# Kernel optimization log

Measured on AMD Instinct MI355X. Metric: run time of the kernel, lower is better.

The kernel has to match this reference:

```python
import jax, jax.numpy as jnp
import numpy as np

NUM_LEVELS = 3
B, T, D, H = 512, 2048, 64, 32


def _uni(k, shape, fan_in):
    s = 1.0 / np.sqrt(fan_in)
    return jax.random.uniform(k, shape, jnp.float32, -s, s)


def setup_inputs() -> dict:
    key = jax.random.key(0)
    ks = jax.random.split(key, 10)
    lw = jnp.linspace(1.0, float(NUM_LEVELS), NUM_LEVELS)
    lw = lw / lw.sum()
    return {
        "latent_ys": jax.random.normal(ks[0], (B, T, D), jnp.float32),
        "Wx": _uni(ks[1], (D, H), D), "bx": _uni(ks[2], (H,), D),
        "Wu": _uni(ks[3], (D, H), D), "bu": _uni(ks[4], (H,), D),
        "Ws": _uni(ks[5], (2 * H, 1), 2 * H), "bs": _uni(ks[6], (1,), 2 * H),
        "level_weights": lw,
        "Wf": _uni(ks[7], (2 * D, D), 2 * D), "bf": _uni(ks[8], (D,), 2 * D),
        "gamma": jnp.ones((D,), jnp.float32),
        "beta": jnp.zeros((D,), jnp.float32),
    }


def reference(latent_ys, Wx, bx, Wu, bu, Ws, bs, level_weights, Wf, bf, gamma, beta):
    Bn, Tn, Dn = latent_ys.shape
    x_repr = latent_ys[:, 0, :]          # (B,D)
    u_repr = latent_ys.mean(axis=1)       # (B,D)

    # Eq. 8-9 attention: score_net is linear on concat, so S[i,j] = ex_i.w1 + eu_j.w2 + b
    ex = x_repr @ Wx + bx                 # (B,H)
    eu = u_repr @ Wu + bu                 # (B,H)
    Hn = ex.shape[-1]
    S = (ex @ Ws[:Hn, 0])[:, None] + (eu @ Ws[Hn:, 0])[None, :] + bs[0]
    eye = jnp.eye(Bn, dtype=bool)
    S = jnp.where(eye, -jnp.inf, S)
    weights = jax.nn.softmax(S, axis=-1)  # (B,B), diag = 0

    # pyramidal sort (Algorithm 1), vectorized over the batch dim
    other = ~eye
    active = other
    dt = latent_ys.dtype
    levels = []
    for _ in range(NUM_LEVELS - 1):
        cnt = active.sum(-1, keepdims=True).astype(dt)                         # (B,1)
        asum = jnp.sum(jnp.where(active, weights, 0.0), -1, keepdims=True)      # (B,1)
        mean_val = asum / jnp.maximum(cnt, 1.0)
        lower = active & (weights <= mean_val)                                  # (B,B)
        lcnt = lower.sum(-1).astype(dt)[:, None]                                # (B,1)
        lsum = lower.astype(dt) @ u_repr                                        # (B,D)
        levels.append(jnp.where(lcnt > 0, lsum / jnp.maximum(lcnt, 1.0), 0.0))
        active = active & ~lower
    acnt = active.sum(-1).astype(dt)[:, None]
    asum_r = active.astype(dt) @ u_repr
    top_idx = jnp.argmax(jnp.where(other, weights, -1.0), axis=-1)              # (B,)
    fallback = u_repr[top_idx]
    levels.append(jnp.where(acnt > 0, asum_r / jnp.maximum(acnt, 1.0), fallback))
    level_reprs = jnp.stack(levels, axis=1)                                     # (B,L,D)

    cross = jnp.einsum('bld,l->bd', level_reprs, level_weights)                 # (B,D)
    # fusion Linear on concat([latent_ys, cross]) split into two GEMMs
    fused = latent_ys @ Wf[:Dn] + (cross @ Wf[Dn:] + bf)[:, None, :]           # (B,T,D)
    y = fused + latent_ys
    mu = y.mean(-1, keepdims=True)
    var = y.var(-1, keepdims=True)
    return gamma * (y - mu) * jax.lax.rsqrt(var + 1e-5) + beta
```

## Files before the change

### kernel.cpp

```cpp
#include <hip/hip_runtime.h>

typedef unsigned short ushort_t;
typedef __attribute__((ext_vector_type(8))) short short8;
typedef __attribute__((ext_vector_type(4))) float f32x4;

#define BB 512
#define TT 2048
#define DD 64

__device__ __forceinline__ ushort_t f2b(float f) {
    union { float f; unsigned int i; } v; v.f = f;
    unsigned int u = v.i;
    unsigned int r = (u + 0x7fffu + ((u >> 16) & 1u)) >> 16;
    return (ushort_t)r;
}

__global__ __launch_bounds__(1024) void k_umean(const float* __restrict__ lat,
                                                const float* __restrict__ Wu,
                                                const float* __restrict__ Ws,
                                                float* __restrict__ u,
                                                float* __restrict__ bj,
                                                ushort_t* __restrict__ latb) {
    int b = blockIdx.x;
    int tid = threadIdx.x;
    int cg = tid & 15;
    int rs = tid >> 4;
    const float* base = lat + (size_t)b * TT * DD;
    ushort_t* bbase = latb + (size_t)b * TT * DD;
    float acc[4] = {0.f, 0.f, 0.f, 0.f};
#pragma unroll 4
    for (int k = 0; k < 32; k++) {
        int r = rs + 64 * k;
        float4 vv = *reinterpret_cast<const float4*>(base + (size_t)r * DD + cg * 4);
        acc[0] += vv.x; acc[1] += vv.y; acc[2] += vv.z; acc[3] += vv.w;
        ushort4 sv;
        sv.x = f2b(vv.x); sv.y = f2b(vv.y); sv.z = f2b(vv.z); sv.w = f2b(vv.w);
        *reinterpret_cast<ushort4*>(bbase + (size_t)r * DD + cg * 4) = sv;
    }
    __shared__ float sm[64][64];
#pragma unroll
    for (int j = 0; j < 4; j++) sm[rs][cg * 4 + j] = acc[j];
    __syncthreads();
    {
        int col = tid & 63, g = tid >> 6;
        float p = 0.0f;
#pragma unroll
        for (int k = 0; k < 4; k++) p += sm[g + 16 * k][col];
        sm[g][col] = p;
    }
    __syncthreads();
    if (tid < 64) {
        float tot = 0.0f;
#pragma unroll
        for (int g = 0; g < 16; g++) tot += sm[g][tid];
        float um = tot * (1.0f / (float)TT);
        u[(size_t)b * DD + tid] = um;
        float vv = 0.0f;
#pragma unroll
        for (int h = 0; h < 32; h++) vv += Wu[tid * 32 + h] * Ws[32 + h];
        float p = um * vv;
#pragma unroll
        for (int m = 1; m < 64; m <<= 1) p += __shfl_xor(p, m, 64);
        if (tid == 0) bj[b] = p;
    }
}

__global__ __launch_bounds__(256) void k_levels(const float* __restrict__ u,
                                                const float* __restrict__ bj,
                                                const float* __restrict__ lw,
                                                const float* __restrict__ Wf,
                                                const float* __restrict__ bfv,
                                                float* __restrict__ cbias) {
    int i = blockIdx.x;
    int tid = threadIdx.x;
    int lane = tid & 63, wv = tid >> 6;
    __shared__ signed char lvl[512];
    __shared__ float redf[16];
    __shared__ int redi[8];
    __shared__ __align__(16) float lr[16][3][64];
    __shared__ float crossS[64];

    int jA = tid, jB = tid + 256;
    float vA = bj[jA], vB = bj[jB];

    float mx; int mi;
    if (vB > vA) { mx = vB; mi = jB; } else { mx = vA; mi = jA; }
#pragma unroll
    for (int m = 1; m < 64; m <<= 1) {
        float om = __shfl_xor(mx, m, 64);
        int oi = __shfl_xor(mi, m, 64);
        if (om > mx || (om == mx && oi < mi)) { mx = om; mi = oi; }
    }
    if (lane == 0) { redf[wv] = mx; redi[wv] = mi; }
    __syncthreads();
    float maxb = redf[0]; int j1 = redi[0];
#pragma unroll
    for (int w2 = 1; w2 < 4; w2++) {
        float om = redf[w2]; int oi = redi[w2];
        if (om > maxb || (om == maxb && oi < j1)) { maxb = om; j1 = oi; }
    }

    float eA = expf(vA - maxb), eB = expf(vB - maxb);
    float zs = eA + eB;
    float mx2; int mi2;
    {
        float tA = (jA == j1) ? -3.4e38f : vA;
        float tB = (jB == j1) ? -3.4e38f : vB;
        if (tB > tA) { mx2 = tB; mi2 = jB; } else { mx2 = tA; mi2 = jA; }
    }
#pragma unroll
    for (int m = 1; m < 64; m <<= 1) {
        float om = __shfl_xor(mx2, m, 64);
        int oi = __shfl_xor(mi2, m, 64);
        if (om > mx2 || (om == mx2 && oi < mi2)) { mx2 = om; mi2 = oi; }
        zs += __shfl_xor(zs, m, 64);
    }
    if (lane == 0) { redf[4 + wv] = mx2; redi[4 + wv] = mi2; redf[8 + wv] = zs; }
    __syncthreads();
    float Z = redf[8] + redf[9] + redf[10] + redf[11];
    int j2 = redi[4]; float m2v = redf[4];
#pragma unroll
    for (int w2 = 1; w2 < 4; w2++) {
        float om = redf[4 + w2]; int oi = redi[4 + w2];
        if (om > m2v || (om == m2v && oi < j2)) { m2v = om; j2 = oi; }
    }

    float Ei = expf(bj[i] - maxb);
    float denom = Z - Ei;
    float wA = (jA == i) ? 0.0f : (eA / denom);
    float wB = (jB == i) ? 0.0f : (eB / denom);

    float s = wA + wB;
#pragma unroll
    for (int m = 1; m < 64; m <<= 1) s += __shfl_xor(s, m, 64);
    if (lane == 0) redf[wv] = s;
    __syncthreads();
    float mean0 = (redf[0] + redf[1] + redf[2] + redf[3]) * (1.0f / 511.0f);

    float pa = 0.0f, ca = 0.0f, c1 = 0.0f;
    if (jA != i) { if (wA <= mean0) c1 += 1.0f; else { pa += wA; ca += 1.0f; } }
    if (jB != i) { if (wB <= mean0) c1 += 1.0f; else { pa += wB; ca += 1.0f; } }
#pragma unroll
    for (int m = 1; m < 64; m <<= 1) {
        pa += __shfl_xor(pa, m, 64);
        ca += __shfl_xor(ca, m, 64);
        c1 += __shfl_xor(c1, m, 64);
    }
    if (lane == 0) { redf[4 + wv] = pa; redf[8 + wv] = ca; redf[12 + wv] = c1; }
    __syncthreads();
    float asum1 = redf[4] + redf[5] + redf[6] + redf[7];
    float cact  = redf[8] + redf[9] + redf[10] + redf[11];
    float cnt1  = redf[12] + redf[13] + redf[14] + redf[15];
    float mean1 = asum1 / fmaxf(cact, 1.0f);

    float c2 = 0.0f;
    signed char lA, lB;
    if (jA == i) lA = -1;
    else if (wA <= mean0) lA = 0;
    else if (wA <= mean1) { lA = 1; c2 += 1.0f; }
    else lA = 2;
    if (jB == i) lB = -1;
    else if (wB <= mean0) lB = 0;
    else if (wB <= mean1) { lB = 1; c2 += 1.0f; }
    else lB = 2;
    lvl[jA] = lA; lvl[jB] = lB;
#pragma unroll
    for (int m = 1; m < 64; m <<= 1) c2 += __shfl_xor(c2, m, 64);
    if (lane == 0) redf[wv] = c2;
    __syncthreads();
    float cnt2 = redf[0] + redf[1] + redf[2] + redf[3];
    float cnt3 = cact - cnt2;

    int jg = tid >> 4;
    int d4 = (tid & 15) << 2;
    float4 a0 = make_float4(0.f, 0.f, 0.f, 0.f);
    float4 a1 = make_float4(0.f, 0.f, 0.f, 0.f);
    float4 a2 = make_float4(0.f, 0.f, 0.f, 0.f);
#pragma unroll 8
    for (int j = jg; j < 512; j += 16) {
        int l = lvl[j];
        float4 uv = *reinterpret_cast<const float4*>(u + (size_t)j * DD + d4);
        if (l == 0) { a0.x += uv.x; a0.y += uv.y; a0.z += uv.z; a0.w += uv.w; }
        else if (l == 1) { a1.x += uv.x; a1.y += uv.y; a1.z += uv.z; a1.w += uv.w; }
        else if (l == 2) { a2.x += uv.x; a2.y += uv.y; a2.z += uv.z; a2.w += uv.w; }
    }
    *reinterpret_cast<float4*>(&lr[jg][0][d4]) = a0;
    *reinterpret_cast<float4*>(&lr[jg][1][d4]) = a1;
    *reinterpret_cast<float4*>(&lr[jg][2][d4]) = a2;
    __syncthreads();

    if (tid < 64) {
        float s0 = 0.0f, s1 = 0.0f, s2 = 0.0f;
#pragma unroll
        for (int g2 = 0; g2 < 16; g2++) {
            s0 += lr[g2][0][tid];
            s1 += lr[g2][1][tid];
            s2 += lr[g2][2][tid];
        }
        int fb = (j1 == i) ? j2 : j1;
        float L1 = (cnt1 > 0.0f) ? s0 / cnt1 : 0.0f;
        float L2 = (cnt2 > 0.0f) ? s1 / cnt2 : 0.0f;
        float L3 = (cnt3 > 0.0f) ? s2 / cnt3 : u[(size_t)fb * DD + tid];
        crossS[tid] = lw[0] * L1 + lw[1] * L2 + lw[2] * L3;
    }
    __syncthreads();
    if (tid < 64) {
        int n = tid;
        float sacc = 0.0f;
        for (int dd = 0; dd < 64; dd++) sacc += crossS[dd] * Wf[(64 + dd) * 64 + n];
        cbias[(size_t)i * DD + n] = sacc + bfv[n];
    }
}

__global__ __launch_bounds__(256) void k_fused(const ushort_t* __restrict__ latb,
                                               const float* __restrict__ Wf,
                                               const float* __restrict__ cbias,
                                               const float* __restrict__ gamma,
                                               const float* __restrict__ beta,
                                               float* __restrict__ out) {
    int tid = threadIdx.x;
    int lane = tid & 63, wv = tid >> 6;
    int lo = lane & 15, quad = lane >> 4;
    long wid = (long)blockIdx.x * 4 + wv;

    short8 bfr[4][2];
#pragma unroll
    for (int c = 0; c < 4; c++) {
        int n = 16 * c + lo;
#pragma unroll
        for (int s = 0; s < 2; s++) {
            short8 t;
#pragma unroll
            for (int j = 0; j < 8; j++) {
                int k = 32 * s + 8 * quad + j;
                float vv = Wf[k * 64 + n] + (k == n ? 1.0f : 0.0f);
                t[j] = (short)f2b(vv);
            }
            bfr[c][s] = t;
        }
    }
    float ga[4], be[4], cb[4];
    int b = (int)(wid >> 5);
#pragma unroll
    for (int c = 0; c < 4; c++) {
        int n = 16 * c + lo;
        ga[c] = gamma[n];
        be[c] = beta[n];
        cb[c] = cbias[(size_t)b * DD + n];
    }

    for (int t4 = 0; t4 < 4; t4++) {
        long row0 = (wid * 4 + t4) * 16;
        const ushort_t* ap = latb + (size_t)(row0 + lo) * DD + quad * 8;
        short8 a0 = *reinterpret_cast<const short8*>(ap);
        short8 a1 = *reinterpret_cast<const short8*>(ap + 32);

        f32x4 acc[4];
#pragma unroll
        for (int c = 0; c < 4; c++) { acc[c] = (f32x4){0.f, 0.f, 0.f, 0.f}; }
#pragma unroll
        for (int c = 0; c < 4; c++) {
            acc[c] = __builtin_amdgcn_mfma_f32_16x16x32_bf16(a0, bfr[c][0], acc[c], 0, 0, 0);
            acc[c] = __builtin_amdgcn_mfma_f32_16x16x32_bf16(a1, bfr[c][1], acc[c], 0, 0, 0);
        }
        float y[4][4];
#pragma unroll
        for (int c = 0; c < 4; c++)
#pragma unroll
            for (int r = 0; r < 4; r++) y[c][r] = acc[c][r] + cb[c];
#pragma unroll
        for (int r = 0; r < 4; r++) {
            float s = y[0][r] + y[1][r] + y[2][r] + y[3][r];
            float q = y[0][r] * y[0][r] + y[1][r] * y[1][r] + y[2][r] * y[2][r] + y[3][r] * y[3][r];
#pragma unroll
            for (int m = 1; m < 16; m <<= 1) {
                s += __shfl_xor(s, m, 64);
                q += __shfl_xor(q, m, 64);
            }
            float mean = s * (1.0f / 64.0f);
            float var = q * (1.0f / 64.0f) - mean * mean;
            float rstd = rsqrtf(var + 1e-5f);
            long row = row0 + quad * 4 + r;
#pragma unroll
            for (int c = 0; c < 4; c++) {
                float o = ga[c] * (y[c][r] - mean) * rstd + be[c];
                out[(size_t)row * DD + 16 * c + lo] = o;
            }
        }
    }
}

extern "C" void kernel_launch(void* const* d_in, const int* in_sizes, int n_in,
                              void* d_out, int out_size, void* d_ws, size_t ws_size,
                              hipStream_t stream) {
    const float* lat   = (const float*)d_in[0];
    const float* Wu    = (const float*)d_in[3];
    const float* Ws    = (const float*)d_in[5];
    const float* lw    = (const float*)d_in[7];
    const float* Wf    = (const float*)d_in[8];
    const float* bfv   = (const float*)d_in[9];
    const float* gamma = (const float*)d_in[10];
    const float* beta  = (const float*)d_in[11];
    float* out = (float*)d_out;

    char* ws = (char*)d_ws;
    float*    u     = (float*)(ws);
    float*    bjv   = (float*)(ws + 131072);
    float*    cbias = (float*)(ws + 133120);
    ushort_t* latb  = (ushort_t*)(ws + 264192);

    k_umean<<<BB, 1024, 0, stream>>>(lat, Wu, Ws, u, bjv, latb);
    k_levels<<<BB, 256, 0, stream>>>(u, bjv, lw, Wf, bfv, cbias);
    k_fused<<<4096, 256, 0, stream>>>(latb, Wf, cbias, gamma, beta, out);
}
```

Baseline: 554.2 us.

## Drop bf16 staging copy; read fp32 input directly in fused GEMM kernel

The first kernel no longer writes a bf16 copy of the full input to workspace. The fused GEMM+LayerNorm kernel now reads the fp32 input directly and converts it to bf16 in registers. Blocks walk the rows in reverse order so that the most recently read rows, likely still in the last-level cache, are reused first. Output stores become nontemporal. Together these remove a 128 MB write plus a 128 MB read, in exchange for reading 256 MB of fp32 in the GEMM kernel.

```diff
diff --git a/kernel.cpp b/kernel.cpp
--- a/kernel.cpp
+++ b/kernel.cpp
@@ -19,23 +19,18 @@
                                                 const float* __restrict__ Wu,
                                                 const float* __restrict__ Ws,
                                                 float* __restrict__ u,
-                                                float* __restrict__ bj,
-                                                ushort_t* __restrict__ latb) {
+                                                float* __restrict__ bj) {
     int b = blockIdx.x;
     int tid = threadIdx.x;
     int cg = tid & 15;
     int rs = tid >> 4;
     const float* base = lat + (size_t)b * TT * DD;
-    ushort_t* bbase = latb + (size_t)b * TT * DD;
     float acc[4] = {0.f, 0.f, 0.f, 0.f};
 #pragma unroll 4
     for (int k = 0; k < 32; k++) {
         int r = rs + 64 * k;
         float4 vv = *reinterpret_cast<const float4*>(base + (size_t)r * DD + cg * 4);
         acc[0] += vv.x; acc[1] += vv.y; acc[2] += vv.z; acc[3] += vv.w;
-        ushort4 sv;
-        sv.x = f2b(vv.x); sv.y = f2b(vv.y); sv.z = f2b(vv.z); sv.w = f2b(vv.w);
-        *reinterpret_cast<ushort4*>(bbase + (size_t)r * DD + cg * 4) = sv;
     }
     __shared__ float sm[64][64];
 #pragma unroll
@@ -212,7 +207,7 @@
     }
 }
 
-__global__ __launch_bounds__(256) void k_fused(const ushort_t* __restrict__ latb,
+__global__ __launch_bounds__(256) void k_fused(const float* __restrict__ lat,
                                                const float* __restrict__ Wf,
                                                const float* __restrict__ cbias,
                                                const float* __restrict__ gamma,
@@ -221,7 +216,7 @@
     int tid = threadIdx.x;
     int lane = tid & 63, wv = tid >> 6;
     int lo = lane & 15, quad = lane >> 4;
-    long wid = (long)blockIdx.x * 4 + wv;
+    long wid = 16383 - ((long)blockIdx.x * 4 + wv);
 
     short8 bfr[4][2];
 #pragma unroll
@@ -251,9 +246,20 @@
 
     for (int t4 = 0; t4 < 4; t4++) {
         long row0 = (wid * 4 + t4) * 16;
-        const ushort_t* ap = latb + (size_t)(row0 + lo) * DD + quad * 8;
-        short8 a0 = *reinterpret_cast<const short8*>(ap);
-        short8 a1 = *reinterpret_cast<const short8*>(ap + 32);
+        const float* ap = lat + (size_t)(row0 + lo) * DD + quad * 8;
+        float4 f0 = *reinterpret_cast<const float4*>(ap);
+        float4 f1 = *reinterpret_cast<const float4*>(ap + 4);
+        float4 f2 = *reinterpret_cast<const float4*>(ap + 32);
+        float4 f3 = *reinterpret_cast<const float4*>(ap + 36);
+        short8 a0, a1;
+        a0[0] = (short)f2b(f0.x); a0[1] = (short)f2b(f0.y);
+        a0[2] = (short)f2b(f0.z); a0[3] = (short)f2b(f0.w);
+        a0[4] = (short)f2b(f1.x); a0[5] = (short)f2b(f1.y);
+        a0[6] = (short)f2b(f1.z); a0[7] = (short)f2b(f1.w);
+        a1[0] = (short)f2b(f2.x); a1[1] = (short)f2b(f2.y);
+        a1[2] = (short)f2b(f2.z); a1[3] = (short)f2b(f2.w);
+        a1[4] = (short)f2b(f3.x); a1[5] = (short)f2b(f3.y);
+        a1[6] = (short)f2b(f3.z); a1[7] = (short)f2b(f3.w);
 
         f32x4 acc[4];
 #pragma unroll
@@ -284,7 +290,7 @@
 #pragma unroll
             for (int c = 0; c < 4; c++) {
                 float o = ga[c] * (y[c][r] - mean) * rstd + be[c];
-                out[(size_t)row * DD + 16 * c + lo] = o;
+                __builtin_nontemporal_store(o, &out[(size_t)row * DD + 16 * c + lo]);
             }
         }
     }
@@ -304,12 +310,11 @@
     float* out = (float*)d_out;
 
     char* ws = (char*)d_ws;
-    float*    u     = (float*)(ws);
-    float*    bjv   = (float*)(ws + 131072);
-    float*    cbias = (float*)(ws + 133120);
-    ushort_t* latb  = (ushort_t*)(ws + 264192);
-
-    k_umean<<<BB, 1024, 0, stream>>>(lat, Wu, Ws, u, bjv, latb);
+    float* u     = (float*)(ws);
+    float* bjv   = (float*)(ws + 131072);
+    float* cbias = (float*)(ws + 133120);
+
+    k_umean<<<BB, 1024, 0, stream>>>(lat, Wu, Ws, u, bjv);
     k_levels<<<BB, 256, 0, stream>>>(u, bjv, lw, Wf, bfv, cbias);
-    k_fused<<<4096, 256, 0, stream>>>(latb, Wf, cbias, gamma, beta, out);
-}
+    k_fused<<<4096, 256, 0, stream>>>(lat, Wf, cbias, gamma, beta, out);
+}
```

Measured after the change: 524.0 us. 1.06x faster.
